# Performance work log

Measured on AMD Instinct MI355X. Metric: run time of the kernel, lower is better.

## Reference

```python
import jax, jax.numpy as jnp
import numpy as np

B, C, H, W_, N, E = 8, 256, 128, 128, 4096, 128
EPS = 1e-12  # torch F.normalize default eps


def grid_sample_points(x, kpts):
    """Bilinear grid_sample at point coords, padding_mode='zeros', align_corners=False.
    x: [B,C,H,W], kpts: [B,N,2] in [-1,1] (x,y order) -> [B,C,N].
    """
    Bx, Cx, Hx, Wx = x.shape
    # unnormalize (align_corners=False)
    ix = (kpts[..., 0] + 1.0) * (Wx * 0.5) - 0.5  # [B,N]
    iy = (kpts[..., 1] + 1.0) * (Hx * 0.5) - 0.5
    x0f = jnp.floor(ix)
    y0f = jnp.floor(iy)
    wx = ix - x0f  # fractional weights
    wy = iy - y0f
    x0 = x0f.astype(jnp.int32)
    y0 = y0f.astype(jnp.int32)
    x1 = x0 + 1
    y1 = y0 + 1

    def gather(xi, yi):
        valid = (xi >= 0) & (xi < Wx) & (yi >= 0) & (yi < Hx)  # [B,N]
        xc = jnp.clip(xi, 0, Wx - 1)
        yc = jnp.clip(yi, 0, Hx - 1)
        # per-batch gather of [C] vectors at N points -> [B,C,N]
        v = jax.vmap(lambda xb, yy, xx: xb[:, yy, xx])(x, yc, xc)
        return v * valid[:, None, :].astype(x.dtype)

    v00 = gather(x0, y0)
    v10 = gather(x1, y0)
    v01 = gather(x0, y1)
    v11 = gather(x1, y1)
    wxb = wx[:, None, :]
    wyb = wy[:, None, :]
    return (v00 * (1 - wxb) * (1 - wyb)
            + v10 * wxb * (1 - wyb)
            + v01 * (1 - wxb) * wyb
            + v11 * wxb * wyb)


def setup_inputs() -> dict:
    key = jax.random.key(0)
    k1, k2, k3 = jax.random.split(key, 3)
    x = jax.random.normal(k1, (B, C, H, W_), dtype=jnp.float32)
    # keypoints in normalized [-1,1] coords (grid_sample convention)
    kpts = jax.random.uniform(k2, (B, N, 2), dtype=jnp.float32) * 2.0 - 1.0
    # xavier_normal_(gain=0.1) for Linear(C -> E)
    std = 0.1 * np.sqrt(2.0 / (C + E))
    whiten_w = jax.random.normal(k3, (E, C), dtype=jnp.float32) * std
    whiten_b = jnp.zeros((E,), dtype=jnp.float32)
    return {"x": x, "kpts": kpts, "whiten_w": whiten_w, "whiten_b": whiten_b}


def reference(x, kpts, whiten_w, whiten_b):
    desc = grid_sample_points(x, kpts)              # [B,C,N]
    desc = jnp.transpose(desc, (0, 2, 1))           # [B,N,C]
    desc = jnp.einsum('bnc,ec->bne', desc, whiten_w) + whiten_b  # [B,N,E]
    norm = jnp.maximum(jnp.linalg.norm(desc, axis=2, keepdims=True), EPS)
    return desc / norm
```

## Files before the change

### kernel.cpp

```cpp
#include <hip/hip_runtime.h>
#include <hip/hip_bf16.h>
#include <math.h>

#define BB 8
#define CC 256
#define HH 128
#define WW 128
#define NN 4096
#define EE 128

#define WT_OFF   0
#define BASE_OFF 131072
#define WGT_OFF  262144
#define DESC_OFF 786432
#define WS_NEED  (786432ull + (unsigned long long)BB*CC*NN*4ull)

__global__ __launch_bounds__(256) void prep_kernel(
    const float* __restrict__ kpts, const float* __restrict__ W,
    int* __restrict__ baseb, float4* __restrict__ wgt, float* __restrict__ Wt) {
  int i = blockIdx.x * blockDim.x + threadIdx.x;
  int c = i >> 7, e = i & (EE - 1);
  Wt[i] = W[e * CC + c];
  float kx = kpts[2 * i], ky = kpts[2 * i + 1];
  float ix = (kx + 1.f) * (WW * 0.5f) - 0.5f;
  float iy = (ky + 1.f) * (HH * 0.5f) - 0.5f;
  float x0f = floorf(ix), y0f = floorf(iy);
  float wx = ix - x0f, wy = iy - y0f;
  int x0 = (int)x0f, y0 = (int)y0f;
  float ax0 = (x0 >= 0 && x0 < WW) ? (1.f - wx) : 0.f;
  float ax1 = (x0 + 1 >= 0 && x0 + 1 < WW) ? wx : 0.f;
  float ay0 = (y0 >= 0 && y0 < HH) ? (1.f - wy) : 0.f;
  float ay1 = (y0 + 1 >= 0 && y0 + 1 < HH) ? wy : 0.f;
  int bx = min(max(x0, 0), WW - 2);
  int by = min(max(y0, 0), HH - 2);
  float a0 = 0.f, a1 = 0.f, c0 = 0.f, c1 = 0.f;
  if (x0 == bx) a0 += ax0; else if (x0 == bx + 1) a1 += ax0;
  if (x0 + 1 == bx) a0 += ax1; else if (x0 + 1 == bx + 1) a1 += ax1;
  if (y0 == by) c0 += ay0; else if (y0 == by + 1) c1 += ay0;
  if (y0 + 1 == by) c0 += ay1; else if (y0 + 1 == by + 1) c1 += ay1;
  baseb[i] = by * WW + bx;
  wgt[i] = make_float4(a0 * c0, a1 * c0, a0 * c1, a1 * c1);
}

__global__ __launch_bounds__(512) void gather_kernel(
    const float* __restrict__ x, const int* __restrict__ baseb,
    const float4* __restrict__ wgt, float* __restrict__ desc) {
  __shared__ float plane[HH * WW];
  int blk = blockIdx.x;
  int b = blk >> 8;
  int t = threadIdx.x;
  const float4* s4 = (const float4*)(x + ((size_t)blk << 14));
  float4* p4 = (float4*)plane;
#pragma unroll
  for (int i = 0; i < 8; ++i) p4[t + 512 * i] = s4[t + 512 * i];
  __syncthreads();
  const int* bb = baseb + b * NN;
  const float4* wb = wgt + b * NN;
  float* dst = desc + ((size_t)blk << 12);
#pragma unroll
  for (int i = 0; i < 8; ++i) {
    int n = t + 512 * i;
    int base = bb[n];
    float4 w = wb[n];
    dst[n] = plane[base] * w.x + plane[base + 1] * w.y
           + plane[base + WW] * w.z + plane[base + WW + 1] * w.w;
  }
}

__global__ __launch_bounds__(512) void gemm_norm_kernel(
    const float* __restrict__ desc, const float* __restrict__ Wt,
    const float* __restrict__ bias, float* __restrict__ out) {
  __shared__ float4 A4s[32 * 16];
  __shared__ float4 W4s[32 * 32];
  int t = threadIdx.x;
  int blk = blockIdx.x;
  int b = blk >> 6;
  int n0 = (blk & 63) << 6;
  int te = t & 31;
  int tn = t >> 5;
  float acc[4][4];
#pragma unroll
  for (int j = 0; j < 4; ++j)
#pragma unroll
    for (int k = 0; k < 4; ++k) acc[j][k] = 0.f;
  const float4* wt4 = (const float4*)Wt;
  const float4* d4 = (const float4*)desc;
  for (int cb = 0; cb < CC; cb += 32) {
    __syncthreads();
    int base4 = (b * CC + cb) * (NN / 4) + (n0 >> 2);
    {
      int ccA = t >> 4, iiA = t & 15;
      A4s[t] = d4[base4 + ccA * (NN / 4) + iiA];
    }
#pragma unroll
    for (int p = 0; p < 2; ++p) {
      int q = t + 512 * p;
      int cc = q >> 5, ii = q & 31;
      W4s[q] = wt4[(cb + cc) * (EE / 4) + ii];
    }
    __syncthreads();
#pragma unroll
    for (int cc = 0; cc < 32; ++cc) {
      float4 a = A4s[cc * 16 + tn];
      float4 w = W4s[cc * 32 + te];
      float av[4] = {a.x, a.y, a.z, a.w};
      float wv[4] = {w.x, w.y, w.z, w.w};
#pragma unroll
      for (int j = 0; j < 4; ++j)
#pragma unroll
        for (int k = 0; k < 4; ++k) acc[j][k] += wv[j] * av[k];
    }
  }
  float4 bi = ((const float4*)bias)[te];
  float bv[4] = {bi.x, bi.y, bi.z, bi.w};
#pragma unroll
  for (int j = 0; j < 4; ++j)
#pragma unroll
    for (int k = 0; k < 4; ++k) acc[j][k] += bv[j];
  float4* out4 = (float4*)out;
#pragma unroll
  for (int k = 0; k < 4; ++k) {
    float s = 0.f;
#pragma unroll
    for (int j = 0; j < 4; ++j) s += acc[j][k] * acc[j][k];
    s += __shfl_xor(s, 1); s += __shfl_xor(s, 2); s += __shfl_xor(s, 4);
    s += __shfl_xor(s, 8); s += __shfl_xor(s, 16);
    float inv = 1.f / fmaxf(sqrtf(s), 1e-12f);
    int n = n0 + tn * 4 + k;
    out4[((size_t)(b * NN + n) << 5) + te] =
        make_float4(acc[0][k] * inv, acc[1][k] * inv, acc[2][k] * inv, acc[3][k] * inv);
  }
}

__global__ __launch_bounds__(128) void fused_fallback(
    const float* __restrict__ x, const float* __restrict__ kpts,
    const float* __restrict__ W, const float* __restrict__ bias,
    float* __restrict__ out) {
  __shared__ float dsc[CC];
  __shared__ float sred[2];
  int blk = blockIdx.x;
  int b = blk >> 12;
  float kx = kpts[2 * blk], ky = kpts[2 * blk + 1];
  float ix = (kx + 1.f) * (WW * 0.5f) - 0.5f;
  float iy = (ky + 1.f) * (HH * 0.5f) - 0.5f;
  float x0f = floorf(ix), y0f = floorf(iy);
  float wx = ix - x0f, wy = iy - y0f;
  int x0 = (int)x0f, y0 = (int)y0f;
  float ax0 = (x0 >= 0 && x0 < WW) ? (1.f - wx) : 0.f;
  float ax1 = (x0 + 1 >= 0 && x0 + 1 < WW) ? wx : 0.f;
  float ay0 = (y0 >= 0 && y0 < HH) ? (1.f - wy) : 0.f;
  float ay1 = (y0 + 1 >= 0 && y0 + 1 < HH) ? wy : 0.f;
  int bx = min(max(x0, 0), WW - 2);
  int by = min(max(y0, 0), HH - 2);
  float a0 = 0.f, a1 = 0.f, r0 = 0.f, r1 = 0.f;
  if (x0 == bx) a0 += ax0; else if (x0 == bx + 1) a1 += ax0;
  if (x0 + 1 == bx) a0 += ax1; else if (x0 + 1 == bx + 1) a1 += ax1;
  if (y0 == by) r0 += ay0; else if (y0 == by + 1) r1 += ay0;
  if (y0 + 1 == by) r0 += ay1; else if (y0 + 1 == by + 1) r1 += ay1;
  int base = by * WW + bx;
  float w00 = a0 * r0, w10 = a1 * r0, w01 = a0 * r1, w11 = a1 * r1;
  int t = threadIdx.x;
  const float* src = x + ((size_t)b << 22);
  for (int c = t; c < CC; c += 128) {
    const float* p = src + ((size_t)c << 14);
    dsc[c] = p[base] * w00 + p[base + 1] * w10 + p[base + WW] * w01 + p[base + WW + 1] * w11;
  }
  __syncthreads();
  float acc = bias[t];
  const float* wr = W + t * CC;
  for (int c = 0; c < CC; ++c) acc += wr[c] * dsc[c];
  float s = acc * acc;
  for (int m = 1; m < 64; m <<= 1) s += __shfl_xor(s, m);
  if ((t & 63) == 0) sred[t >> 6] = s;
  __syncthreads();
  float tot = sred[0] + sred[1];
  float inv = 1.f / fmaxf(sqrtf(tot), 1e-12f);
  out[((size_t)blk << 7) + t] = acc * inv;
}

extern "C" void kernel_launch(void* const* d_in, const int* in_sizes, int n_in,
                              void* d_out, int out_size, void* d_ws, size_t ws_size,
                              hipStream_t stream) {
  const float* x    = (const float*)d_in[0];
  const float* kpts = (const float*)d_in[1];
  const float* W    = (const float*)d_in[2];
  const float* bias = (const float*)d_in[3];
  float* out = (float*)d_out;
  if (ws_size >= WS_NEED) {
    char* ws = (char*)d_ws;
    float* Wt    = (float*)(ws + WT_OFF);
    int* baseb   = (int*)(ws + BASE_OFF);
    float4* wgt  = (float4*)(ws + WGT_OFF);
    float* desc  = (float*)(ws + DESC_OFF);
    prep_kernel<<<BB * NN / 256, 256, 0, stream>>>(kpts, W, baseb, wgt, Wt);
    gather_kernel<<<BB * CC, 512, 0, stream>>>(x, baseb, wgt, desc);
    gemm_norm_kernel<<<BB * (NN / 64), 512, 0, stream>>>(desc, Wt, bias, out);
  } else {
    fused_fallback<<<BB * NN, 128, 0, stream>>>(x, kpts, W, bias, out);
  }
}
```

Before: 233.1 us.

## Use bf16 MFMA for whitening GEMM with fragment-ordered intermediate layout

The gather kernel now writes the sampled descriptors as bf16 in a layout already matched to MFMA B-fragments, and prep stores the weight matrix as bf16 in A-fragment order. The GEMM+normalize kernel becomes a 16x16x32 bf16 MFMA kernel: each wave handles 16 points, keeps the whole weight matrix in LDS and reduces the norm with shuffles. This halves the intermediate traffic and moves the FP32 FMA inner loop onto matrix cores, at the cost of bf16 rounding in inputs to the projection.

```diff
diff --git a/kernel.cpp b/kernel.cpp
--- a/kernel.cpp
+++ b/kernel.cpp
@@ -9,18 +9,25 @@
 #define NN 4096
 #define EE 128
 
-#define WT_OFF   0
-#define BASE_OFF 131072
-#define WGT_OFF  262144
-#define DESC_OFF 786432
-#define WS_NEED  (786432ull + (unsigned long long)BB*CC*NN*4ull)
+typedef __bf16 bf16x8 __attribute__((ext_vector_type(8)));
+typedef float f32x4 __attribute__((ext_vector_type(4)));
+
+#define WF_OFF    0
+#define BASE_OFF  65536
+#define WGT_OFF   196608
+#define DESCF_OFF 720896
+#define WS_NEED   (720896ull + 16777216ull)
 
 __global__ __launch_bounds__(256) void prep_kernel(
     const float* __restrict__ kpts, const float* __restrict__ W,
-    int* __restrict__ baseb, float4* __restrict__ wgt, float* __restrict__ Wt) {
+    int* __restrict__ baseb, float4* __restrict__ wgt, __bf16* __restrict__ Wf) {
   int i = blockIdx.x * blockDim.x + threadIdx.x;
-  int c = i >> 7, e = i & (EE - 1);
-  Wt[i] = W[e * CC + c];
+  {
+    int j = i & 7, lane = (i >> 3) & 63, etile = (i >> 9) & 7, kstep = (i >> 12) & 7;
+    int e = etile * 16 + (lane & 15);
+    int c = kstep * 32 + ((lane >> 4) << 3) + j;
+    Wf[i] = (__bf16)W[e * CC + c];
+  }
   float kx = kpts[2 * i], ky = kpts[2 * i + 1];
   float ix = (kx + 1.f) * (WW * 0.5f) - 0.5f;
   float iy = (ky + 1.f) * (HH * 0.5f) - 0.5f;
@@ -44,10 +51,10 @@
 
 __global__ __launch_bounds__(512) void gather_kernel(
     const float* __restrict__ x, const int* __restrict__ baseb,
-    const float4* __restrict__ wgt, float* __restrict__ desc) {
+    const float4* __restrict__ wgt, __bf16* __restrict__ descf) {
   __shared__ float plane[HH * WW];
   int blk = blockIdx.x;
-  int b = blk >> 8;
+  int b = blk >> 8, c = blk & 255;
   int t = threadIdx.x;
   const float4* s4 = (const float4*)(x + ((size_t)blk << 14));
   float4* p4 = (float4*)plane;
@@ -56,80 +63,71 @@
   __syncthreads();
   const int* bb = baseb + b * NN;
   const float4* wb = wgt + b * NN;
-  float* dst = desc + ((size_t)blk << 12);
+  __bf16* dst = descf + ((b << 20) + ((c >> 5) << 9) + (((c >> 3) & 3) << 7) + (c & 7));
 #pragma unroll
   for (int i = 0; i < 8; ++i) {
     int n = t + 512 * i;
     int base = bb[n];
     float4 w = wb[n];
-    dst[n] = plane[base] * w.x + plane[base + 1] * w.y
-           + plane[base + WW] * w.z + plane[base + WW + 1] * w.w;
+    float v = plane[base] * w.x + plane[base + 1] * w.y
+            + plane[base + WW] * w.z + plane[base + WW + 1] * w.w;
+    dst[((n >> 4) << 12) + ((n & 15) << 3)] = (__bf16)v;
   }
 }
 
-__global__ __launch_bounds__(512) void gemm_norm_kernel(
-    const float* __restrict__ desc, const float* __restrict__ Wt,
+__global__ __launch_bounds__(256) void gemm_norm_kernel(
+    const __bf16* __restrict__ descf, const __bf16* __restrict__ Wf,
     const float* __restrict__ bias, float* __restrict__ out) {
-  __shared__ float4 A4s[32 * 16];
-  __shared__ float4 W4s[32 * 32];
+  __shared__ __bf16 wlds[8 * 8 * 64 * 8];
   int t = threadIdx.x;
+  {
+    const float4* src = (const float4*)Wf;
+    float4* d = (float4*)wlds;
+#pragma unroll
+    for (int i = 0; i < 16; ++i) d[t + 256 * i] = src[t + 256 * i];
+  }
+  __syncthreads();
   int blk = blockIdx.x;
   int b = blk >> 6;
-  int n0 = (blk & 63) << 6;
-  int te = t & 31;
-  int tn = t >> 5;
-  float acc[4][4];
+  int wave = t >> 6, lane = t & 63;
+  int ntile = ((blk & 63) << 2) + wave;
+  const bf16x8* bsrc =
+      (const bf16x8*)(descf + ((size_t)b << 20) + ((size_t)ntile << 12));
+  bf16x8 bfrag[8];
 #pragma unroll
-  for (int j = 0; j < 4; ++j)
+  for (int k = 0; k < 8; ++k) bfrag[k] = bsrc[k * 64 + lane];
+  const bf16x8* alds = (const bf16x8*)wlds;
+  f32x4 acc[8];
 #pragma unroll
-    for (int k = 0; k < 4; ++k) acc[j][k] = 0.f;
-  const float4* wt4 = (const float4*)Wt;
-  const float4* d4 = (const float4*)desc;
-  for (int cb = 0; cb < CC; cb += 32) {
-    __syncthreads();
-    int base4 = (b * CC + cb) * (NN / 4) + (n0 >> 2);
-    {
-      int ccA = t >> 4, iiA = t & 15;
-      A4s[t] = d4[base4 + ccA * (NN / 4) + iiA];
-    }
+  for (int e = 0; e < 8; ++e) acc[e] = (f32x4)(0.f);
 #pragma unroll
-    for (int p = 0; p < 2; ++p) {
-      int q = t + 512 * p;
-      int cc = q >> 5, ii = q & 31;
-      W4s[q] = wt4[(cb + cc) * (EE / 4) + ii];
-    }
-    __syncthreads();
+  for (int k = 0; k < 8; ++k) {
 #pragma unroll
-    for (int cc = 0; cc < 32; ++cc) {
-      float4 a = A4s[cc * 16 + tn];
-      float4 w = W4s[cc * 32 + te];
-      float av[4] = {a.x, a.y, a.z, a.w};
-      float wv[4] = {w.x, w.y, w.z, w.w};
-#pragma unroll
-      for (int j = 0; j < 4; ++j)
-#pragma unroll
-        for (int k = 0; k < 4; ++k) acc[j][k] += wv[j] * av[k];
+    for (int e = 0; e < 8; ++e) {
+      bf16x8 a = alds[(k * 8 + e) * 64 + lane];
+      acc[e] = __builtin_amdgcn_mfma_f32_16x16x32_bf16(a, bfrag[k], acc[e], 0, 0, 0);
     }
   }
-  float4 bi = ((const float4*)bias)[te];
-  float bv[4] = {bi.x, bi.y, bi.z, bi.w};
+  int quad = lane >> 4, col = lane & 15;
+  int n = ntile * 16 + col;
+  float s = 0.f;
+  float4 av[8];
 #pragma unroll
-  for (int j = 0; j < 4; ++j)
+  for (int e = 0; e < 8; ++e) {
+    float4 bi = *(const float4*)(bias + e * 16 + quad * 4);
+    float4 v = make_float4(acc[e][0] + bi.x, acc[e][1] + bi.y,
+                           acc[e][2] + bi.z, acc[e][3] + bi.w);
+    av[e] = v;
+    s += v.x * v.x + v.y * v.y + v.z * v.z + v.w * v.w;
+  }
+  s += __shfl_xor(s, 16);
+  s += __shfl_xor(s, 32);
+  float inv = 1.f / fmaxf(sqrtf(s), 1e-12f);
+  float4* out4 = (float4*)out + (((size_t)(b * NN + n)) << 5) + quad;
 #pragma unroll
-    for (int k = 0; k < 4; ++k) acc[j][k] += bv[j];
-  float4* out4 = (float4*)out;
-#pragma unroll
-  for (int k = 0; k < 4; ++k) {
-    float s = 0.f;
-#pragma unroll
-    for (int j = 0; j < 4; ++j) s += acc[j][k] * acc[j][k];
-    s += __shfl_xor(s, 1); s += __shfl_xor(s, 2); s += __shfl_xor(s, 4);
-    s += __shfl_xor(s, 8); s += __shfl_xor(s, 16);
-    float inv = 1.f / fmaxf(sqrtf(s), 1e-12f);
-    int n = n0 + tn * 4 + k;
-    out4[((size_t)(b * NN + n) << 5) + te] =
-        make_float4(acc[0][k] * inv, acc[1][k] * inv, acc[2][k] * inv, acc[3][k] * inv);
-  }
+  for (int e = 0; e < 8; ++e)
+    out4[e * 4] = make_float4(av[e].x * inv, av[e].y * inv,
+                              av[e].z * inv, av[e].w * inv);
 }
 
 __global__ __launch_bounds__(128) void fused_fallback(
@@ -188,13 +186,13 @@
   float* out = (float*)d_out;
   if (ws_size >= WS_NEED) {
     char* ws = (char*)d_ws;
-    float* Wt    = (float*)(ws + WT_OFF);
-    int* baseb   = (int*)(ws + BASE_OFF);
-    float4* wgt  = (float4*)(ws + WGT_OFF);
-    float* desc  = (float*)(ws + DESC_OFF);
-    prep_kernel<<<BB * NN / 256, 256, 0, stream>>>(kpts, W, baseb, wgt, Wt);
-    gather_kernel<<<BB * CC, 512, 0, stream>>>(x, baseb, wgt, desc);
-    gemm_norm_kernel<<<BB * (NN / 64), 512, 0, stream>>>(desc, Wt, bias, out);
+    __bf16* Wf    = (__bf16*)(ws + WF_OFF);
+    int* baseb    = (int*)(ws + BASE_OFF);
+    float4* wgt   = (float4*)(ws + WGT_OFF);
+    __bf16* descf = (__bf16*)(ws + DESCF_OFF);
+    prep_kernel<<<BB * NN / 256, 256, 0, stream>>>(kpts, W, baseb, wgt, Wf);
+    gather_kernel<<<BB * CC, 512, 0, stream>>>(x, baseb, wgt, descf);
+    gemm_norm_kernel<<<BB * (NN / 64), 256, 0, stream>>>(descf, Wf, bias, out);
   } else {
     fused_fallback<<<BB * NN, 128, 0, stream>>>(x, kpts, W, bias, out);
   }
```

After: 222.1 us. 4.7% less time.
